# Performance work log

Hardware: AMD Instinct MI355X
Metric: run time of the kernel (lower is better)

The kernel has to match this reference:

```python
import jax, jax.numpy as jnp
import numpy as np

BS, N, DE, DX = 16, 256, 64, 256
BIG = 100000.0


def setup_inputs() -> dict:
    key = jax.random.key(0)
    k1, k2, k3, k4 = jax.random.split(key, 4)
    E = jax.random.normal(k1, (BS, N, N, DE), dtype=jnp.float32)
    e_mask2 = jax.random.uniform(k2, (BS, 1, N, 1)) < 0.8
    fan_in = 4 * DE
    bound = 1.0 / np.sqrt(fan_in)
    W = jax.random.uniform(k3, (DX, fan_in), minval=-bound, maxval=bound, dtype=jnp.float32)
    b = jax.random.uniform(k4, (DX,), minval=-bound, maxval=bound, dtype=jnp.float32)
    return {"E": E, "e_mask2": e_mask2, "W": W, "b": b}


def reference(E, e_mask2, W, b):
    bs, n, _, de = E.shape
    mask = jnp.broadcast_to(e_mask2, (bs, n, n, de)).astype(E.dtype)  # bs,n,n,de
    imask = 1.0 - mask
    denom = mask.sum(axis=2)                       # bs,n,de
    m = E.sum(axis=2) / denom                      # (faithful: unmasked sum / mask count)
    mi = (E + BIG * imask).min(axis=2)             # masked min
    ma = (E - BIG * imask).max(axis=2)             # masked max
    std = (((E - m[:, :, None, :]) ** 2) * mask).sum(axis=2) / denom
    z = jnp.concatenate((m, mi, ma, std), axis=2)  # bs,n,4*de
    return jnp.einsum('bnf,df->bnd', z, W) + b     # bs,n,dx
```

## Files before the change

### kernel.cpp

```cpp
#include <hip/hip_runtime.h>
#include <cstdint>
#include <cstddef>

#define BSZ 16
#define NN  256
#define DE  64
#define DXX 256
#define IB  4

__global__ __launch_bounds__(256, 4) void etox_fused(
    const float* __restrict__ E, const uint8_t* __restrict__ raw,
    const float* __restrict__ W, const float* __restrict__ bias,
    float* __restrict__ out)
{
    __shared__ float m_lds[NN];
    __shared__ int   det[2];
    __shared__ float cpart[4];
    __shared__ float partial[4][16][20];
    __shared__ float z_lds[IB][4 * DE];

    const int t   = threadIdx.x;
    const int g0  = blockIdx.x * IB;
    const int b   = g0 >> 8;

    if (t == 0) { det[0] = 0; det[1] = 0; }
    int s1 = 0, s23 = 0;
    {
        const uint8_t* p = raw + t * 16;
        #pragma unroll
        for (int u = 0; u < 16; ++u) {
            int v = (int)p[u];
            int m4 = u & 3;
            if (m4 == 1) s1 += v; else if (m4 >= 2) s23 += v;
        }
    }
    __syncthreads();
    if (s1)  atomicAdd(&det[0], s1);
    if (s23) atomicAdd(&det[1], s23);
    __syncthreads();
    const int kind = (det[1] == 0) ? 1 : ((det[0] == 0) ? 2 : 0);

    float mv;
    {
        int idx = b * NN + t;
        if (kind == 1)      mv = (((const int*)(const void*)raw)[idx] != 0) ? 1.f : 0.f;
        else if (kind == 2) mv = (((const float*)(const void*)raw)[idx] != 0.f) ? 1.f : 0.f;
        else                mv = (raw[idx] != 0) ? 1.f : 0.f;
    }
    m_lds[t] = mv;
    unsigned long long bal = __ballot(mv != 0.f);
    const int wv = t >> 6, lane = t & 63;
    if (lane == 0) cpart[wv] = (float)__popcll(bal);
    __syncthreads();
    const float inv_cnt = 1.0f / (cpart[0] + cpart[1] + cpart[2] + cpart[3]);

    const int dq = t & 15;
    const int jb = t >> 4;
    const float* base0 = E + (size_t)g0 * (NN * DE) + (size_t)jb * DE + 4 * dq;

    #define LD(P, K) (*(const float4*)((P) + (size_t)(K) * (16 * DE)))
    float4 A0, A1, A2, A3, B0, B1, B2, B3;
    A0 = LD(base0, 0); A1 = LD(base0, 1); A2 = LD(base0, 2); A3 = LD(base0, 3);

    for (int r = 0; r < IB; ++r) {
        const float* baser = base0 + (size_t)r * (NN * DE);

        float s[4]  = {0.f, 0.f, 0.f, 0.f};
        float ms[4] = {0.f, 0.f, 0.f, 0.f};
        float q[4]  = {0.f, 0.f, 0.f, 0.f};
        float mi[4] = {1e30f, 1e30f, 1e30f, 1e30f};
        float ma[4] = {-1e30f, -1e30f, -1e30f, -1e30f};

        #define CONS1(V, KK) { \
            float mk = m_lds[jb + 16 * (KK)]; \
            bool on = (mk != 0.f); \
            float4 v = V; \
            s[0] += v.x; s[1] += v.y; s[2] += v.z; s[3] += v.w; \
            ms[0] = fmaf(mk, v.x, ms[0]); ms[1] = fmaf(mk, v.y, ms[1]); \
            ms[2] = fmaf(mk, v.z, ms[2]); ms[3] = fmaf(mk, v.w, ms[3]); \
            q[0] = fmaf(mk * v.x, v.x, q[0]); q[1] = fmaf(mk * v.y, v.y, q[1]); \
            q[2] = fmaf(mk * v.z, v.z, q[2]); q[3] = fmaf(mk * v.w, v.w, q[3]); \
            mi[0] = fminf(mi[0], on ? v.x : 1e30f); mi[1] = fminf(mi[1], on ? v.y : 1e30f); \
            mi[2] = fminf(mi[2], on ? v.z : 1e30f); mi[3] = fminf(mi[3], on ? v.w : 1e30f); \
            ma[0] = fmaxf(ma[0], on ? v.x : -1e30f); ma[1] = fmaxf(ma[1], on ? v.y : -1e30f); \
            ma[2] = fmaxf(ma[2], on ? v.z : -1e30f); ma[3] = fmaxf(ma[3], on ? v.w : -1e30f); \
        }

        B0 = LD(baser, 4);  B1 = LD(baser, 5);  B2 = LD(baser, 6);  B3 = LD(baser, 7);
        CONS1(A0, 0) CONS1(A1, 1) CONS1(A2, 2) CONS1(A3, 3)
        A0 = LD(baser, 8);  A1 = LD(baser, 9);  A2 = LD(baser, 10); A3 = LD(baser, 11);
        CONS1(B0, 4) CONS1(B1, 5) CONS1(B2, 6) CONS1(B3, 7)
        B0 = LD(baser, 12); B1 = LD(baser, 13); B2 = LD(baser, 14); B3 = LD(baser, 15);
        CONS1(A0, 8) CONS1(A1, 9) CONS1(A2, 10) CONS1(A3, 11)
        if (r < IB - 1) {
            const float* basen = baser + (NN * DE);
            A0 = LD(basen, 0); A1 = LD(basen, 1); A2 = LD(basen, 2); A3 = LD(basen, 3);
        }
        CONS1(B0, 12) CONS1(B1, 13) CONS1(B2, 14) CONS1(B3, 15)
        #undef CONS1

        #pragma unroll
        for (int c = 0; c < 4; ++c) {
            s[c]  += __shfl_xor(s[c], 16);  s[c]  += __shfl_xor(s[c], 32);
            ms[c] += __shfl_xor(ms[c], 16); ms[c] += __shfl_xor(ms[c], 32);
            q[c]  += __shfl_xor(q[c], 16);  q[c]  += __shfl_xor(q[c], 32);
            mi[c] = fminf(mi[c], __shfl_xor(mi[c], 16));
            mi[c] = fminf(mi[c], __shfl_xor(mi[c], 32));
            ma[c] = fmaxf(ma[c], __shfl_xor(ma[c], 16));
            ma[c] = fmaxf(ma[c], __shfl_xor(ma[c], 32));
        }

        if (lane < 16) {
            float* p = partial[wv][lane];
            #pragma unroll
            for (int c = 0; c < 4; ++c) {
                p[c]      = s[c];
                p[4 + c]  = ms[c];
                p[8 + c]  = q[c];
                p[12 + c] = mi[c];
                p[16 + c] = ma[c];
            }
        }
        __syncthreads();

        if (t < 64) {
            const int d = t, dq2 = d >> 2, c = d & 3;
            float ss = 0.f, mss = 0.f, mq = 0.f, lmi = 1e30f, lma = -1e30f;
            #pragma unroll
            for (int w = 0; w < 4; ++w) {
                const float* p = partial[w][dq2];
                ss  += p[c];
                mss += p[4 + c];
                mq  += p[8 + c];
                lmi  = fminf(lmi, p[12 + c]);
                lma  = fmaxf(lma, p[16 + c]);
            }
            float m    = ss * inv_cnt;
            float stdv = mq * inv_cnt - 2.0f * m * (mss * inv_cnt) + m * m;
            z_lds[r][d]       = m;
            z_lds[r][64 + d]  = lmi;
            z_lds[r][128 + d] = lma;
            z_lds[r][192 + d] = stdv;
        }
        __syncthreads();
    }
    #undef LD

    float acc0, acc1, acc2, acc3;
    {
        float bv = bias[t];
        acc0 = bv; acc1 = bv; acc2 = bv; acc3 = bv;
    }
    const float4* Wrow = (const float4*)(W + (size_t)t * 4 * DE);
    #pragma unroll 8
    for (int f4 = 0; f4 < 64; ++f4) {
        float4 w4 = Wrow[f4];
        int f = 4 * f4;
        acc0 += z_lds[0][f] * w4.x + z_lds[0][f+1] * w4.y + z_lds[0][f+2] * w4.z + z_lds[0][f+3] * w4.w;
        acc1 += z_lds[1][f] * w4.x + z_lds[1][f+1] * w4.y + z_lds[1][f+2] * w4.z + z_lds[1][f+3] * w4.w;
        acc2 += z_lds[2][f] * w4.x + z_lds[2][f+1] * w4.y + z_lds[2][f+2] * w4.z + z_lds[2][f+3] * w4.w;
        acc3 += z_lds[3][f] * w4.x + z_lds[3][f+1] * w4.y + z_lds[3][f+2] * w4.z + z_lds[3][f+3] * w4.w;
    }
    out[(size_t)(g0 + 0) * DXX + t] = acc0;
    out[(size_t)(g0 + 1) * DXX + t] = acc1;
    out[(size_t)(g0 + 2) * DXX + t] = acc2;
    out[(size_t)(g0 + 3) * DXX + t] = acc3;
}

extern "C" void kernel_launch(void* const* d_in, const int* in_sizes, int n_in,
                              void* d_out, int out_size, void* d_ws, size_t ws_size,
                              hipStream_t stream) {
    const float*   E    = (const float*)d_in[0];
    const uint8_t* mraw = (const uint8_t*)d_in[1];
    const float*   W    = (const float*)d_in[2];
    const float*   bias = (const float*)d_in[3];
    float*         out  = (float*)d_out;

    etox_fused<<<(BSZ * NN) / IB, 256, 0, stream>>>(E, mraw, W, bias, out);
}
```

Before: 71.39 us.

## Assign one wave per output row to drop cross-wave LDS reductions and barriers

Each of the four wavefronts now reduces one full row of 256 neighbours on its own, instead of all four waves sharing each row and combining partials through shared memory with two barriers per row. This removes the partial-sum LDS buffer, the per-row syncthreads and the single-wave combine step, leaving one barrier before the matvec. The masked min and max now use fma with the reference's BIG offset rather than a select. Each wave runs a longer serial loop of loads, and the four waves no longer share a single row's cache lines.

```diff
diff --git a/kernel.cpp b/kernel.cpp
--- a/kernel.cpp
+++ b/kernel.cpp
@@ -7,6 +7,7 @@
 #define DE  64
 #define DXX 256
 #define IB  4
+#define BIGF 100000.0f
 
 __global__ __launch_bounds__(256, 4) void etox_fused(
     const float* __restrict__ E, const uint8_t* __restrict__ raw,
@@ -16,12 +17,13 @@
     __shared__ float m_lds[NN];
     __shared__ int   det[2];
     __shared__ float cpart[4];
-    __shared__ float partial[4][16][20];
     __shared__ float z_lds[IB][4 * DE];
 
-    const int t   = threadIdx.x;
-    const int g0  = blockIdx.x * IB;
-    const int b   = g0 >> 8;
+    const int t    = threadIdx.x;
+    const int g0   = blockIdx.x * IB;
+    const int b    = g0 >> 8;
+    const int wv   = t >> 6;
+    const int lane = t & 63;
 
     if (t == 0) { det[0] = 0; det[1] = 0; }
     int s1 = 0, s23 = 0;
@@ -49,102 +51,80 @@
     }
     m_lds[t] = mv;
     unsigned long long bal = __ballot(mv != 0.f);
-    const int wv = t >> 6, lane = t & 63;
     if (lane == 0) cpart[wv] = (float)__popcll(bal);
     __syncthreads();
     const float inv_cnt = 1.0f / (cpart[0] + cpart[1] + cpart[2] + cpart[3]);
 
-    const int dq = t & 15;
-    const int jb = t >> 4;
-    const float* base0 = E + (size_t)g0 * (NN * DE) + (size_t)jb * DE + 4 * dq;
+    const int dq = lane & 15;
+    const int jb = lane >> 4;
+    const float* rbase = E + (size_t)(g0 + wv) * (NN * DE) + (size_t)jb * DE + 4 * dq;
 
-    #define LD(P, K) (*(const float4*)((P) + (size_t)(K) * (16 * DE)))
+    #define LD(K) (*(const float4*)(rbase + (size_t)(K) * (4 * DE)))
+
+    float s0=0.f,s1_=0.f,s2=0.f,s3=0.f;
+    float ms0=0.f,ms1=0.f,ms2=0.f,ms3=0.f;
+    float q0=0.f,q1=0.f,q2=0.f,q3=0.f;
+    float mi0=1e30f,mi1=1e30f,mi2=1e30f,mi3=1e30f;
+    float ma0=-1e30f,ma1=-1e30f,ma2=-1e30f,ma3=-1e30f;
+
+    #define CONS(V, KK) { \
+        float mk = m_lds[jb + 4 * (KK)]; \
+        float im = 1.0f - mk; \
+        float4 v = V; \
+        s0 += v.x; s1_ += v.y; s2 += v.z; s3 += v.w; \
+        ms0 = fmaf(mk, v.x, ms0); ms1 = fmaf(mk, v.y, ms1); \
+        ms2 = fmaf(mk, v.z, ms2); ms3 = fmaf(mk, v.w, ms3); \
+        q0 = fmaf(mk * v.x, v.x, q0); q1 = fmaf(mk * v.y, v.y, q1); \
+        q2 = fmaf(mk * v.z, v.z, q2); q3 = fmaf(mk * v.w, v.w, q3); \
+        mi0 = fminf(mi0, fmaf(im,  BIGF, v.x)); mi1 = fminf(mi1, fmaf(im,  BIGF, v.y)); \
+        mi2 = fminf(mi2, fmaf(im,  BIGF, v.z)); mi3 = fminf(mi3, fmaf(im,  BIGF, v.w)); \
+        ma0 = fmaxf(ma0, fmaf(im, -BIGF, v.x)); ma1 = fmaxf(ma1, fmaf(im, -BIGF, v.y)); \
+        ma2 = fmaxf(ma2, fmaf(im, -BIGF, v.z)); ma3 = fmaxf(ma3, fmaf(im, -BIGF, v.w)); \
+    }
+
     float4 A0, A1, A2, A3, B0, B1, B2, B3;
-    A0 = LD(base0, 0); A1 = LD(base0, 1); A2 = LD(base0, 2); A3 = LD(base0, 3);
+    A0 = LD(0); A1 = LD(1); A2 = LD(2); A3 = LD(3);
 
-    for (int r = 0; r < IB; ++r) {
-        const float* baser = base0 + (size_t)r * (NN * DE);
+    #pragma unroll 1
+    for (int k = 0; k < 56; k += 8) {
+        B0 = LD(k + 4); B1 = LD(k + 5); B2 = LD(k + 6); B3 = LD(k + 7);
+        CONS(A0, k + 0) CONS(A1, k + 1) CONS(A2, k + 2) CONS(A3, k + 3)
+        A0 = LD(k + 8); A1 = LD(k + 9); A2 = LD(k + 10); A3 = LD(k + 11);
+        CONS(B0, k + 4) CONS(B1, k + 5) CONS(B2, k + 6) CONS(B3, k + 7)
+    }
+    B0 = LD(60); B1 = LD(61); B2 = LD(62); B3 = LD(63);
+    CONS(A0, 56) CONS(A1, 57) CONS(A2, 58) CONS(A3, 59)
+    CONS(B0, 60) CONS(B1, 61) CONS(B2, 62) CONS(B3, 63)
+    #undef CONS
+    #undef LD
 
-        float s[4]  = {0.f, 0.f, 0.f, 0.f};
-        float ms[4] = {0.f, 0.f, 0.f, 0.f};
-        float q[4]  = {0.f, 0.f, 0.f, 0.f};
-        float mi[4] = {1e30f, 1e30f, 1e30f, 1e30f};
-        float ma[4] = {-1e30f, -1e30f, -1e30f, -1e30f};
+    #define RED_ADD(x) { x += __shfl_xor(x, 16); x += __shfl_xor(x, 32); }
+    #define RED_MIN(x) { x = fminf(x, __shfl_xor(x, 16)); x = fminf(x, __shfl_xor(x, 32)); }
+    #define RED_MAX(x) { x = fmaxf(x, __shfl_xor(x, 16)); x = fmaxf(x, __shfl_xor(x, 32)); }
+    RED_ADD(s0) RED_ADD(s1_) RED_ADD(s2) RED_ADD(s3)
+    RED_ADD(ms0) RED_ADD(ms1) RED_ADD(ms2) RED_ADD(ms3)
+    RED_ADD(q0) RED_ADD(q1) RED_ADD(q2) RED_ADD(q3)
+    RED_MIN(mi0) RED_MIN(mi1) RED_MIN(mi2) RED_MIN(mi3)
+    RED_MAX(ma0) RED_MAX(ma1) RED_MAX(ma2) RED_MAX(ma3)
+    #undef RED_ADD
+    #undef RED_MIN
+    #undef RED_MAX
 
-        #define CONS1(V, KK) { \
-            float mk = m_lds[jb + 16 * (KK)]; \
-            bool on = (mk != 0.f); \
-            float4 v = V; \
-            s[0] += v.x; s[1] += v.y; s[2] += v.z; s[3] += v.w; \
-            ms[0] = fmaf(mk, v.x, ms[0]); ms[1] = fmaf(mk, v.y, ms[1]); \
-            ms[2] = fmaf(mk, v.z, ms[2]); ms[3] = fmaf(mk, v.w, ms[3]); \
-            q[0] = fmaf(mk * v.x, v.x, q[0]); q[1] = fmaf(mk * v.y, v.y, q[1]); \
-            q[2] = fmaf(mk * v.z, v.z, q[2]); q[3] = fmaf(mk * v.w, v.w, q[3]); \
-            mi[0] = fminf(mi[0], on ? v.x : 1e30f); mi[1] = fminf(mi[1], on ? v.y : 1e30f); \
-            mi[2] = fminf(mi[2], on ? v.z : 1e30f); mi[3] = fminf(mi[3], on ? v.w : 1e30f); \
-            ma[0] = fmaxf(ma[0], on ? v.x : -1e30f); ma[1] = fmaxf(ma[1], on ? v.y : -1e30f); \
-            ma[2] = fmaxf(ma[2], on ? v.z : -1e30f); ma[3] = fmaxf(ma[3], on ? v.w : -1e30f); \
+    {
+        float m0 = s0 * inv_cnt, m1 = s1_ * inv_cnt, m2 = s2 * inv_cnt, m3 = s3 * inv_cnt;
+        float sd0 = q0 * inv_cnt - 2.f * m0 * (ms0 * inv_cnt) + m0 * m0;
+        float sd1 = q1 * inv_cnt - 2.f * m1 * (ms1 * inv_cnt) + m1 * m1;
+        float sd2 = q2 * inv_cnt - 2.f * m2 * (ms2 * inv_cnt) + m2 * m2;
+        float sd3 = q3 * inv_cnt - 2.f * m3 * (ms3 * inv_cnt) + m3 * m3;
+        if (lane < 16) {
+            float* zr = z_lds[wv];
+            *(float4*)(zr + 4 * dq)       = make_float4(m0, m1, m2, m3);
+            *(float4*)(zr + 64 + 4 * dq)  = make_float4(mi0, mi1, mi2, mi3);
+            *(float4*)(zr + 128 + 4 * dq) = make_float4(ma0, ma1, ma2, ma3);
+            *(float4*)(zr + 192 + 4 * dq) = make_float4(sd0, sd1, sd2, sd3);
         }
-
-        B0 = LD(baser, 4);  B1 = LD(baser, 5);  B2 = LD(baser, 6);  B3 = LD(baser, 7);
-        CONS1(A0, 0) CONS1(A1, 1) CONS1(A2, 2) CONS1(A3, 3)
-        A0 = LD(baser, 8);  A1 = LD(baser, 9);  A2 = LD(baser, 10); A3 = LD(baser, 11);
-        CONS1(B0, 4) CONS1(B1, 5) CONS1(B2, 6) CONS1(B3, 7)
-        B0 = LD(baser, 12); B1 = LD(baser, 13); B2 = LD(baser, 14); B3 = LD(baser, 15);
-        CONS1(A0, 8) CONS1(A1, 9) CONS1(A2, 10) CONS1(A3, 11)
-        if (r < IB - 1) {
-            const float* basen = baser + (NN * DE);
-            A0 = LD(basen, 0); A1 = LD(basen, 1); A2 = LD(basen, 2); A3 = LD(basen, 3);
-        }
-        CONS1(B0, 12) CONS1(B1, 13) CONS1(B2, 14) CONS1(B3, 15)
-        #undef CONS1
-
-        #pragma unroll
-        for (int c = 0; c < 4; ++c) {
-            s[c]  += __shfl_xor(s[c], 16);  s[c]  += __shfl_xor(s[c], 32);
-            ms[c] += __shfl_xor(ms[c], 16); ms[c] += __shfl_xor(ms[c], 32);
-            q[c]  += __shfl_xor(q[c], 16);  q[c]  += __shfl_xor(q[c], 32);
-            mi[c] = fminf(mi[c], __shfl_xor(mi[c], 16));
-            mi[c] = fminf(mi[c], __shfl_xor(mi[c], 32));
-            ma[c] = fmaxf(ma[c], __shfl_xor(ma[c], 16));
-            ma[c] = fmaxf(ma[c], __shfl_xor(ma[c], 32));
-        }
-
-        if (lane < 16) {
-            float* p = partial[wv][lane];
-            #pragma unroll
-            for (int c = 0; c < 4; ++c) {
-                p[c]      = s[c];
-                p[4 + c]  = ms[c];
-                p[8 + c]  = q[c];
-                p[12 + c] = mi[c];
-                p[16 + c] = ma[c];
-            }
-        }
-        __syncthreads();
-
-        if (t < 64) {
-            const int d = t, dq2 = d >> 2, c = d & 3;
-            float ss = 0.f, mss = 0.f, mq = 0.f, lmi = 1e30f, lma = -1e30f;
-            #pragma unroll
-            for (int w = 0; w < 4; ++w) {
-                const float* p = partial[w][dq2];
-                ss  += p[c];
-                mss += p[4 + c];
-                mq  += p[8 + c];
-                lmi  = fminf(lmi, p[12 + c]);
-                lma  = fmaxf(lma, p[16 + c]);
-            }
-            float m    = ss * inv_cnt;
-            float stdv = mq * inv_cnt - 2.0f * m * (mss * inv_cnt) + m * m;
-            z_lds[r][d]       = m;
-            z_lds[r][64 + d]  = lmi;
-            z_lds[r][128 + d] = lma;
-            z_lds[r][192 + d] = stdv;
-        }
-        __syncthreads();
     }
-    #undef LD
+    __syncthreads();
 
     float acc0, acc1, acc2, acc3;
     {
```

Measured after the change: 74.52 us. 4.4% more time.

## Add prep kernel transposing W and decoding mask, restructure output GEMV

Applied to the files above, without the earlier changes.

A prep kernel transposes W into workspace and decodes the edge mask into floats once, so the main kernel no longer runs per-block mask-format detection. The output projection now splits the fan-in across the four waves, reads coalesced float4 rows of the transposed W, and reduces the partial sums through LDS with a float4 store. This removes the strided per-thread W row reads and the redundant per-block byte scan, at the cost of an extra kernel launch and workspace traffic. A fallback keeps the old path when workspace is too small, and a stray no-op LDS self-assignment was added.

```diff
diff --git a/kernel.cpp b/kernel.cpp
--- a/kernel.cpp
+++ b/kernel.cpp
@@ -6,26 +6,22 @@
 #define NN  256
 #define DE  64
 #define DXX 256
+#define FAN (4 * DE)
 #define IB  4
 
-__global__ __launch_bounds__(256, 4) void etox_fused(
-    const float* __restrict__ E, const uint8_t* __restrict__ raw,
-    const float* __restrict__ W, const float* __restrict__ bias,
-    float* __restrict__ out)
+__global__ __launch_bounds__(256) void prep_kernel(
+    const uint8_t* __restrict__ raw, const float* __restrict__ W,
+    float* __restrict__ WT, float* __restrict__ maskf)
 {
-    __shared__ float m_lds[NN];
-    __shared__ int   det[2];
-    __shared__ float cpart[4];
-    __shared__ float partial[4][16][20];
-    __shared__ float z_lds[IB][4 * DE];
-
     const int t   = threadIdx.x;
-    const int g0  = blockIdx.x * IB;
-    const int b   = g0 >> 8;
-
-    if (t == 0) { det[0] = 0; det[1] = 0; }
-    int s1 = 0, s23 = 0;
-    {
+    const int blk = blockIdx.x;
+    if (blk < FAN) {
+        WT[blk * DXX + t] = W[t * FAN + blk];
+    } else {
+        __shared__ int det[2];
+        if (t == 0) { det[0] = 0; det[1] = 0; }
+        __syncthreads();
+        int s1 = 0, s23 = 0;
         const uint8_t* p = raw + t * 16;
         #pragma unroll
         for (int u = 0; u < 16; ++u) {
@@ -33,15 +29,58 @@
             int m4 = u & 3;
             if (m4 == 1) s1 += v; else if (m4 >= 2) s23 += v;
         }
-    }
-    __syncthreads();
-    if (s1)  atomicAdd(&det[0], s1);
-    if (s23) atomicAdd(&det[1], s23);
-    __syncthreads();
-    const int kind = (det[1] == 0) ? 1 : ((det[0] == 0) ? 2 : 0);
+        if (s1)  atomicAdd(&det[0], s1);
+        if (s23) atomicAdd(&det[1], s23);
+        __syncthreads();
+        const int kind = (det[1] == 0) ? 1 : ((det[0] == 0) ? 2 : 0);
+        for (int idx = t; idx < BSZ * NN; idx += 256) {
+            float mv;
+            if (kind == 1)      mv = (((const int*)(const void*)raw)[idx] != 0) ? 1.f : 0.f;
+            else if (kind == 2) mv = (((const float*)(const void*)raw)[idx] != 0.f) ? 1.f : 0.f;
+            else                mv = (raw[idx] != 0) ? 1.f : 0.f;
+            maskf[idx] = mv;
+        }
+    }
+}
+
+template <bool TR>
+__global__ __launch_bounds__(256, 4) void etox_fused(
+    const float* __restrict__ E, const uint8_t* __restrict__ raw,
+    const float* __restrict__ maskf, const float* __restrict__ W,
+    const float* __restrict__ WT, const float* __restrict__ bias,
+    float* __restrict__ out)
+{
+    __shared__ float  m_lds[NN];
+    __shared__ int    det[2];
+    __shared__ float  cpart[4];
+    __shared__ float  partial[4][16][20];
+    __shared__ float  z_lds[IB][FAN];
+    __shared__ float4 part_c[4][IB][64];
+
+    const int t    = threadIdx.x;
+    const int g0   = blockIdx.x * IB;
+    const int b    = g0 >> 8;
+    const int wv   = t >> 6;
+    const int lane = t & 63;
 
     float mv;
-    {
+    if (TR) {
+        mv = maskf[b * NN + t];
+    } else {
+        if (t == 0) { det[0] = 0; det[1] = 0; }
+        int s1 = 0, s23 = 0;
+        const uint8_t* p = raw + t * 16;
+        #pragma unroll
+        for (int u = 0; u < 16; ++u) {
+            int v = (int)p[u];
+            int m4 = u & 3;
+            if (m4 == 1) s1 += v; else if (m4 >= 2) s23 += v;
+        }
+        __syncthreads();
+        if (s1)  atomicAdd(&det[0], s1);
+        if (s23) atomicAdd(&det[1], s23);
+        __syncthreads();
+        const int kind = (det[1] == 0) ? 1 : ((det[0] == 0) ? 2 : 0);
         int idx = b * NN + t;
         if (kind == 1)      mv = (((const int*)(const void*)raw)[idx] != 0) ? 1.f : 0.f;
         else if (kind == 2) mv = (((const float*)(const void*)raw)[idx] != 0.f) ? 1.f : 0.f;
@@ -49,7 +88,6 @@
     }
     m_lds[t] = mv;
     unsigned long long bal = __ballot(mv != 0.f);
-    const int wv = t >> 6, lane = t & 63;
     if (lane == 0) cpart[wv] = (float)__popcll(bal);
     __syncthreads();
     const float inv_cnt = 1.0f / (cpart[0] + cpart[1] + cpart[2] + cpart[3]);
@@ -137,6 +175,7 @@
             }
             float m    = ss * inv_cnt;
             float stdv = mq * inv_cnt - 2.0f * m * (mss * inv_cnt) + m * m;
+            z_lds[t >> 8][0] = z_lds[t >> 8][0];
             z_lds[r][d]       = m;
             z_lds[r][64 + d]  = lmi;
             z_lds[r][128 + d] = lma;
@@ -146,25 +185,63 @@
     }
     #undef LD
 
-    float acc0, acc1, acc2, acc3;
-    {
-        float bv = bias[t];
-        acc0 = bv; acc1 = bv; acc2 = bv; acc3 = bv;
-    }
-    const float4* Wrow = (const float4*)(W + (size_t)t * 4 * DE);
-    #pragma unroll 8
-    for (int f4 = 0; f4 < 64; ++f4) {
-        float4 w4 = Wrow[f4];
-        int f = 4 * f4;
-        acc0 += z_lds[0][f] * w4.x + z_lds[0][f+1] * w4.y + z_lds[0][f+2] * w4.z + z_lds[0][f+3] * w4.w;
-        acc1 += z_lds[1][f] * w4.x + z_lds[1][f+1] * w4.y + z_lds[1][f+2] * w4.z + z_lds[1][f+3] * w4.w;
-        acc2 += z_lds[2][f] * w4.x + z_lds[2][f+1] * w4.y + z_lds[2][f+2] * w4.z + z_lds[2][f+3] * w4.w;
-        acc3 += z_lds[3][f] * w4.x + z_lds[3][f+1] * w4.y + z_lds[3][f+2] * w4.z + z_lds[3][f+3] * w4.w;
-    }
-    out[(size_t)(g0 + 0) * DXX + t] = acc0;
-    out[(size_t)(g0 + 1) * DXX + t] = acc1;
-    out[(size_t)(g0 + 2) * DXX + t] = acc2;
-    out[(size_t)(g0 + 3) * DXX + t] = acc3;
+    if (TR) {
+        float4 acc[IB];
+        #pragma unroll
+        for (int r = 0; r < IB; ++r) acc[r] = make_float4(0.f, 0.f, 0.f, 0.f);
+
+        const float4* WT4 = (const float4*)WT;
+        int f0 = 64 * wv;
+        #pragma unroll 4
+        for (int fg = 0; fg < 16; ++fg, f0 += 4) {
+            float4 w0 = WT4[(size_t)(f0 + 0) * 64 + lane];
+            float4 w1 = WT4[(size_t)(f0 + 1) * 64 + lane];
+            float4 w2 = WT4[(size_t)(f0 + 2) * 64 + lane];
+            float4 w3 = WT4[(size_t)(f0 + 3) * 64 + lane];
+            #pragma unroll
+            for (int r = 0; r < IB; ++r) {
+                float4 z4 = *(const float4*)(&z_lds[r][f0]);
+                acc[r].x = fmaf(z4.x, w0.x, fmaf(z4.y, w1.x, fmaf(z4.z, w2.x, fmaf(z4.w, w3.x, acc[r].x))));
+                acc[r].y = fmaf(z4.x, w0.y, fmaf(z4.y, w1.y, fmaf(z4.z, w2.y, fmaf(z4.w, w3.y, acc[r].y))));
+                acc[r].z = fmaf(z4.x, w0.z, fmaf(z4.y, w1.z, fmaf(z4.z, w2.z, fmaf(z4.w, w3.z, acc[r].z))));
+                acc[r].w = fmaf(z4.x, w0.w, fmaf(z4.y, w1.w, fmaf(z4.z, w2.w, fmaf(z4.w, w3.w, acc[r].w))));
+            }
+        }
+        #pragma unroll
+        for (int r = 0; r < IB; ++r) part_c[wv][r][lane] = acc[r];
+        __syncthreads();
+
+        const int row = t >> 6, l2 = t & 63;
+        float4 p0 = part_c[0][row][l2], p1 = part_c[1][row][l2];
+        float4 p2 = part_c[2][row][l2], p3 = part_c[3][row][l2];
+        float4 bv = *(const float4*)(bias + 4 * l2);
+        float4 o;
+        o.x = p0.x + p1.x + p2.x + p3.x + bv.x;
+        o.y = p0.y + p1.y + p2.y + p3.y + bv.y;
+        o.z = p0.z + p1.z + p2.z + p3.z + bv.z;
+        o.w = p0.w + p1.w + p2.w + p3.w + bv.w;
+        *(float4*)(out + (size_t)(g0 + row) * DXX + 4 * l2) = o;
+    } else {
+        float acc0, acc1, acc2, acc3;
+        {
+            float bv = bias[t];
+            acc0 = bv; acc1 = bv; acc2 = bv; acc3 = bv;
+        }
+        const float4* Wrow = (const float4*)(W + (size_t)t * FAN);
+        #pragma unroll 8
+        for (int f4 = 0; f4 < 64; ++f4) {
+            float4 w4 = Wrow[f4];
+            int f = 4 * f4;
+            acc0 += z_lds[0][f] * w4.x + z_lds[0][f+1] * w4.y + z_lds[0][f+2] * w4.z + z_lds[0][f+3] * w4.w;
+            acc1 += z_lds[1][f] * w4.x + z_lds[1][f+1] * w4.y + z_lds[1][f+2] * w4.z + z_lds[1][f+3] * w4.w;
+            acc2 += z_lds[2][f] * w4.x + z_lds[2][f+1] * w4.y + z_lds[2][f+2] * w4.z + z_lds[2][f+3] * w4.w;
+            acc3 += z_lds[3][f] * w4.x + z_lds[3][f+1] * w4.y + z_lds[3][f+2] * w4.z + z_lds[3][f+3] * w4.w;
+        }
+        out[(size_t)(g0 + 0) * DXX + t] = acc0;
+        out[(size_t)(g0 + 1) * DXX + t] = acc1;
+        out[(size_t)(g0 + 2) * DXX + t] = acc2;
+        out[(size_t)(g0 + 3) * DXX + t] = acc3;
+    }
 }
 
 extern "C" void kernel_launch(void* const* d_in, const int* in_sizes, int n_in,
@@ -176,5 +253,13 @@
     const float*   bias = (const float*)d_in[3];
     float*         out  = (float*)d_out;
 
-    etox_fused<<<(BSZ * NN) / IB, 256, 0, stream>>>(E, mraw, W, bias, out);
+    const size_t need = (size_t)FAN * DXX * sizeof(float) + (size_t)BSZ * NN * sizeof(float);
+    if (ws_size >= need) {
+        float* WT    = (float*)d_ws;
+        float* maskf = (float*)d_ws + (size_t)FAN * DXX;
+        prep_kernel<<<FAN + 1, 256, 0, stream>>>(mraw, W, WT, maskf);
+        etox_fused<true><<<(BSZ * NN) / IB, 256, 0, stream>>>(E, mraw, maskf, W, WT, bias, out);
+    } else {
+        etox_fused<false><<<(BSZ * NN) / IB, 256, 0, stream>>>(E, mraw, nullptr, W, nullptr, bias, out);
+    }
 }
```

New measurement: 63.53 us. -11.0%, faster.
